# Performance work log

Measured on AMD Instinct MI355X. Metric: run time of the kernel, lower is better.

Reference implementation:

```python
import jax, jax.numpy as jnp
import numpy as np

H, W = 224, 224

def setup_inputs() -> dict:
    key = jax.random.key(0)
    k1, k2, k3 = jax.random.split(key, 3)
    B, C, nPath = 8, 64, 8
    img = jax.random.normal(k1, (B, C, H, W), dtype=jnp.float32)
    hs = jax.random.randint(k2, (nPath, H * W), 0, H, dtype=jnp.int32)
    ws = jax.random.randint(k3, (nPath, H * W), 0, W, dtype=jnp.int32)
    paths = jnp.stack([hs, ws], axis=-1)  # [nPath, H*W, 2]
    return {"img": img, "paths": paths}

def reference(img, paths):
    # img: [B, C, H, W]; paths: [nPath, L, 2] with L = H*W
    B, C = img.shape[0], img.shape[1]
    nPath, L = paths.shape[0], paths.shape[1]
    flat_idx = paths[:, :, 0] * W + paths[:, :, 1]        # [nPath, L]
    img_flat = img.reshape(B, C, H * W)                    # [B, C, H*W]
    # single fused gather: [B, C, nPath, L]
    gathered = jnp.take(img_flat, flat_idx, axis=2)
    # torch.cat along channel dim => [B, nPath*C, L]
    out = jnp.transpose(gathered, (0, 2, 1, 3)).reshape(B, nPath * C, L)
    return out
```

## Files before the change

### kernel.cpp

```cpp
#include <hip/hip_runtime.h>
#include <stdint.h>

typedef float f32x4 __attribute__((ext_vector_type(4)));
typedef unsigned short u16x8 __attribute__((ext_vector_type(8)));

#define HH 224
#define WW 224
#define HWSZ (HH * WW)
#define BB 8
#define CC 64
#define NP 8
#define TL 128
#define LT 64

__device__ __forceinline__ unsigned short f2bf(float f) {
    union { float f; uint32_t u; } cv; cv.f = f;
    uint32_t r = cv.u + 0x7fffu + ((cv.u >> 16) & 1u);
    return (unsigned short)(r >> 16);
}
__device__ __forceinline__ float bf2f(unsigned short us) {
    union { uint32_t u; float f; } cv; cv.u = ((uint32_t)us) << 16;
    return cv.f;
}

__global__ __launch_bounds__(256, 8) void transpose_kernel(const float* __restrict__ img,
                                                           unsigned short* __restrict__ img_tb) {
    __shared__ float lds[CC][LT + 1];
    const int b   = blockIdx.y;
    const int l0  = blockIdx.x * LT;
    const int tid = threadIdx.x;

    const float* src = img + (size_t)b * CC * HWSZ;
    #pragma unroll
    for (int it = 0; it < 4; ++it) {
        const int c = (tid >> 4) + it * 16;
        const int m = tid & 15;
        f32x4 v = __builtin_nontemporal_load(
            reinterpret_cast<const f32x4*>(src + (size_t)c * HWSZ + l0 + 4 * m));
        lds[c][4 * m + 0] = v.x;
        lds[c][4 * m + 1] = v.y;
        lds[c][4 * m + 2] = v.z;
        lds[c][4 * m + 3] = v.w;
    }
    __syncthreads();

    unsigned short* dst = img_tb + (size_t)b * HWSZ * CC;
    #pragma unroll
    for (int it = 0; it < 2; ++it) {
        const int slot = it * 256 + tid;
        const int l    = slot >> 3;
        const int c0   = (slot & 7) << 3;
        u16x8 o;
        #pragma unroll
        for (int j = 0; j < 8; ++j) o[j] = f2bf(lds[c0 + j][l]);
        *reinterpret_cast<u16x8*>(dst + (size_t)(l0 + l) * CC + c0) = o;
    }
}

__global__ __launch_bounds__(512, 8) void gather_kernel(const unsigned short* __restrict__ img_tb,
                                                        const int* __restrict__ paths,
                                                        float* __restrict__ out) {
    __shared__ float tile[CC][TL];
    __shared__ int sidx[TL];

    const int tid = threadIdx.x;
    const int l0  = blockIdx.x * TL;
    const int p   = blockIdx.y;
    const int b   = blockIdx.z;

    if (tid < TL) {
        int2 hw2 = reinterpret_cast<const int2*>(paths)[(size_t)p * HWSZ + l0 + tid];
        sidx[tid] = hw2.x * WW + hw2.y;
    }
    __syncthreads();

    const unsigned short* src = img_tb + (size_t)b * HWSZ * CC;

    #pragma unroll
    for (int it = 0; it < 2; ++it) {
        const int slot = it * 512 + tid;
        const int l    = slot >> 3;
        const int u    = slot & 7;
        const int c0   = u << 3;
        u16x8 v = *reinterpret_cast<const u16x8*>(src + (size_t)sidx[l] * CC + c0);
        const int gA = (((l >> 2) ^ (2 * u)) << 2) + (l & 3);
        const int gB = (((l >> 2) ^ (2 * u + 1)) << 2) + (l & 3);
        tile[c0 + 0][gA] = bf2f(v[0]);
        tile[c0 + 1][gA] = bf2f(v[1]);
        tile[c0 + 2][gA] = bf2f(v[2]);
        tile[c0 + 3][gA] = bf2f(v[3]);
        tile[c0 + 4][gB] = bf2f(v[4]);
        tile[c0 + 5][gB] = bf2f(v[5]);
        tile[c0 + 6][gB] = bf2f(v[6]);
        tile[c0 + 7][gB] = bf2f(v[7]);
    }
    __syncthreads();

    float* dst = out + ((size_t)b * (NP * CC) + (size_t)p * CC) * HWSZ + l0;
    #pragma unroll
    for (int it = 0; it < 4; ++it) {
        const int c = it * 16 + (tid >> 5);
        const int s = tid & 31;
        const int g = (s ^ (c >> 2)) << 2;
        f32x4 v = *reinterpret_cast<const f32x4*>(&tile[c][g]);
        *reinterpret_cast<f32x4*>(dst + (size_t)c * HWSZ + 4 * s) = v;
    }
}

__global__ __launch_bounds__(256) void naive_gather(const float* __restrict__ img,
                                                    const int* __restrict__ paths,
                                                    float* __restrict__ out) {
    const int l = blockIdx.x * 256 + threadIdx.x;
    const int p = blockIdx.y;
    const int b = blockIdx.z;
    int2 hw2 = reinterpret_cast<const int2*>(paths)[(size_t)p * HWSZ + l];
    const int idx = hw2.x * WW + hw2.y;
    const float* src = img + (size_t)b * CC * HWSZ;
    float* dst = out + ((size_t)b * NP + p) * (size_t)(CC * HWSZ) + l;
    #pragma unroll 4
    for (int c = 0; c < CC; ++c) {
        dst[(size_t)c * HWSZ] = src[(size_t)c * HWSZ + idx];
    }
}

extern "C" void kernel_launch(void* const* d_in, const int* in_sizes, int n_in,
                              void* d_out, int out_size, void* d_ws, size_t ws_size,
                              hipStream_t stream) {
    const float* img   = (const float*)d_in[0];
    const int*   paths = (const int*)d_in[1];
    float*       out   = (float*)d_out;

    const size_t need = (size_t)BB * HWSZ * CC * sizeof(unsigned short);
    if (ws_size >= need) {
        unsigned short* img_tb = (unsigned short*)d_ws;
        transpose_kernel<<<dim3(HWSZ / LT, BB), 256, 0, stream>>>(img, img_tb);
        gather_kernel<<<dim3(HWSZ / TL, NP, BB), 512, 0, stream>>>(img_tb, paths, out);
    } else {
        naive_gather<<<dim3(HWSZ / 256, NP, BB), 256, 0, stream>>>(img, paths, out);
    }
}
```

Before: 204.9 us.

## Process four sub-tiles per gather block with register prefetch and nontemporal stores

Each gather block now handles four consecutive 128-position sub-tiles. The gathered bf16 rows for the next sub-tile are loaded into registers while the current tile is written out from LDS, which overlaps gather latency with output stores. Output writes also become nontemporal. In exchange there are four times fewer blocks, the occupancy hint drops, and each sub-tile adds an extra barrier.

```diff
diff --git a/kernel.cpp b/kernel.cpp
--- a/kernel.cpp
+++ b/kernel.cpp
@@ -11,6 +11,8 @@
 #define CC 64
 #define NP 8
 #define TL 128
+#define NSUB 4
+#define SUPER (TL * NSUB)
 #define LT 64
 
 __device__ __forceinline__ unsigned short f2bf(float f) {
@@ -57,53 +59,73 @@
     }
 }
 
-__global__ __launch_bounds__(512, 8) void gather_kernel(const unsigned short* __restrict__ img_tb,
+__global__ __launch_bounds__(512, 4) void gather_kernel(const unsigned short* __restrict__ img_tb,
                                                         const int* __restrict__ paths,
                                                         float* __restrict__ out) {
     __shared__ float tile[CC][TL];
-    __shared__ int sidx[TL];
+    __shared__ int sidx[SUPER];
 
     const int tid = threadIdx.x;
-    const int l0  = blockIdx.x * TL;
+    const int l0  = blockIdx.x * SUPER;
     const int p   = blockIdx.y;
     const int b   = blockIdx.z;
 
-    if (tid < TL) {
+    {
         int2 hw2 = reinterpret_cast<const int2*>(paths)[(size_t)p * HWSZ + l0 + tid];
         sidx[tid] = hw2.x * WW + hw2.y;
     }
     __syncthreads();
 
     const unsigned short* src = img_tb + (size_t)b * HWSZ * CC;
+    float* dst = out + ((size_t)b * (NP * CC) + (size_t)p * CC) * HWSZ + l0;
+
+    const int lA = tid >> 3;
+    const int lB = 64 + lA;
+    const int u  = tid & 7;
+    const int c0 = u << 3;
+    const int gA0 = (((lA >> 2) ^ (2 * u))     << 2) + (lA & 3);
+    const int gA1 = (((lA >> 2) ^ (2 * u + 1)) << 2) + (lA & 3);
+    const int gB0 = (((lB >> 2) ^ (2 * u))     << 2) + (lB & 3);
+    const int gB1 = (((lB >> 2) ^ (2 * u + 1)) << 2) + (lB & 3);
+
+    u16x8 rA = *reinterpret_cast<const u16x8*>(src + (size_t)sidx[lA] * CC + c0);
+    u16x8 rB = *reinterpret_cast<const u16x8*>(src + (size_t)sidx[lB] * CC + c0);
 
     #pragma unroll
-    for (int it = 0; it < 2; ++it) {
-        const int slot = it * 512 + tid;
-        const int l    = slot >> 3;
-        const int u    = slot & 7;
-        const int c0   = u << 3;
-        u16x8 v = *reinterpret_cast<const u16x8*>(src + (size_t)sidx[l] * CC + c0);
-        const int gA = (((l >> 2) ^ (2 * u)) << 2) + (l & 3);
-        const int gB = (((l >> 2) ^ (2 * u + 1)) << 2) + (l & 3);
-        tile[c0 + 0][gA] = bf2f(v[0]);
-        tile[c0 + 1][gA] = bf2f(v[1]);
-        tile[c0 + 2][gA] = bf2f(v[2]);
-        tile[c0 + 3][gA] = bf2f(v[3]);
-        tile[c0 + 4][gB] = bf2f(v[4]);
-        tile[c0 + 5][gB] = bf2f(v[5]);
-        tile[c0 + 6][gB] = bf2f(v[6]);
-        tile[c0 + 7][gB] = bf2f(v[7]);
-    }
-    __syncthreads();
+    for (int sub = 0; sub < NSUB; ++sub) {
+        tile[c0 + 0][gA0] = bf2f(rA[0]);
+        tile[c0 + 1][gA0] = bf2f(rA[1]);
+        tile[c0 + 2][gA0] = bf2f(rA[2]);
+        tile[c0 + 3][gA0] = bf2f(rA[3]);
+        tile[c0 + 4][gA1] = bf2f(rA[4]);
+        tile[c0 + 5][gA1] = bf2f(rA[5]);
+        tile[c0 + 6][gA1] = bf2f(rA[6]);
+        tile[c0 + 7][gA1] = bf2f(rA[7]);
+        tile[c0 + 0][gB0] = bf2f(rB[0]);
+        tile[c0 + 1][gB0] = bf2f(rB[1]);
+        tile[c0 + 2][gB0] = bf2f(rB[2]);
+        tile[c0 + 3][gB0] = bf2f(rB[3]);
+        tile[c0 + 4][gB1] = bf2f(rB[4]);
+        tile[c0 + 5][gB1] = bf2f(rB[5]);
+        tile[c0 + 6][gB1] = bf2f(rB[6]);
+        tile[c0 + 7][gB1] = bf2f(rB[7]);
+        __syncthreads();
 
-    float* dst = out + ((size_t)b * (NP * CC) + (size_t)p * CC) * HWSZ + l0;
-    #pragma unroll
-    for (int it = 0; it < 4; ++it) {
-        const int c = it * 16 + (tid >> 5);
-        const int s = tid & 31;
-        const int g = (s ^ (c >> 2)) << 2;
-        f32x4 v = *reinterpret_cast<const f32x4*>(&tile[c][g]);
-        *reinterpret_cast<f32x4*>(dst + (size_t)c * HWSZ + 4 * s) = v;
+        if (sub + 1 < NSUB) {
+            rA = *reinterpret_cast<const u16x8*>(src + (size_t)sidx[(sub + 1) * TL + lA] * CC + c0);
+            rB = *reinterpret_cast<const u16x8*>(src + (size_t)sidx[(sub + 1) * TL + lB] * CC + c0);
+        }
+
+        #pragma unroll
+        for (int it = 0; it < 4; ++it) {
+            const int c = it * 16 + (tid >> 5);
+            const int s = tid & 31;
+            const int g = (s ^ (c >> 2)) << 2;
+            f32x4 v = *reinterpret_cast<const f32x4*>(&tile[c][g]);
+            __builtin_nontemporal_store(v,
+                reinterpret_cast<f32x4*>(dst + (size_t)c * HWSZ + sub * TL + 4 * s));
+        }
+        __syncthreads();
     }
 }
 
@@ -134,7 +156,7 @@
     if (ws_size >= need) {
         unsigned short* img_tb = (unsigned short*)d_ws;
         transpose_kernel<<<dim3(HWSZ / LT, BB), 256, 0, stream>>>(img, img_tb);
-        gather_kernel<<<dim3(HWSZ / TL, NP, BB), 512, 0, stream>>>(img_tb, paths, out);
+        gather_kernel<<<dim3(HWSZ / SUPER, NP, BB), 512, 0, stream>>>(img_tb, paths, out);
     } else {
         naive_gather<<<dim3(HWSZ / 256, NP, BB), 256, 0, stream>>>(img, paths, out);
     }
```

Measured after the change: 212.9 us. 1.04x slower.
